# Kernel tuning notes

Hardware: AMD Instinct MI355X
Metric: run time of the kernel (lower is better)

Reference implementation:

```python
import jax, jax.numpy as jnp
import numpy as np

B, T, H, V = 64, 512, 300, 50257


def setup_inputs() -> dict:
    key = jax.random.key(0)
    k0, k1, k2, k3, k4 = jax.random.split(key, 5)
    tokens = jax.random.randint(k0, (B, T), 0, V, dtype=jnp.int32)
    ihs = jnp.zeros((B, H), jnp.float32)
    emb = jax.random.normal(k1, (V, H), jnp.float32) * 0.02
    W = jax.random.normal(k2, (H, H), jnp.float32) * (1.0 / np.sqrt(H))
    U = jax.random.normal(k3, (H, H), jnp.float32) * (1.0 / np.sqrt(H))
    Wout = jax.random.normal(k4, (V, H), jnp.float32) * 0.02
    bout = jnp.zeros((V,), jnp.float32)
    return {"ihs": ihs, "tokens": tokens, "emb": emb, "W": W, "U": U,
            "Wout": Wout, "bout": bout}


def reference(ihs, tokens, emb, W, U, Wout, bout):
    # Embedding lookup: [B, T, H]
    x = emb[tokens]
    # Precompute input projection for all timesteps: U x_t (Linear: x @ U^T)
    ux = jnp.einsum('bth,gh->btg', x, U)  # [B, T, H]
    ux_tmajor = jnp.swapaxes(ux, 0, 1)    # [T, B, H]

    def step(h, ux_t):
        # h_t = tanh(W h_{t-1} + U x_t)
        h_next = jnp.tanh(h @ W.T + ux_t)
        return h_next, h_next

    h_last, _ = jax.lax.scan(step, ihs, ux_tmajor)
    # final hidden state -> vocab logits
    logits = h_last @ Wout.T + bout  # [B, V]
    return logits
```

## Files before the change

kernel.cpp:

```cpp
#include <hip/hip_runtime.h>
#include <math.h>

#define H 300
#define BB 64
#define TT 512
#define VV 50257
#define KC 30

__global__ void transpose_k(const float* __restrict__ in, float* __restrict__ out) {
    int idx = blockIdx.x * blockDim.x + threadIdx.x;
    if (idx < H * H) {
        int r = idx / H, c = idx - r * H;
        out[idx] = in[c * H + r];
    }
}

__global__ __launch_bounds__(256) void ux_k(const int* __restrict__ tokens,
                                            const float* __restrict__ emb,
                                            const float* __restrict__ Ut,
                                            float* __restrict__ ux) {
    __shared__ __align__(16) float x_s[KC][BB];
    __shared__ __align__(16) float ut_s[KC][304];
    __shared__ int tok_s[BB];

    const int t = blockIdx.x;
    const int tid = threadIdx.x;
    if (tid < BB) tok_s[tid] = tokens[tid * TT + t];

    const int tb = tid >> 4;
    const int tg = tid & 15;
    const int b0 = tb * 4;
    const int g0 = tg * 20;
    const bool active = (tg < 15);

    float acc[4][20];
#pragma unroll
    for (int i = 0; i < 4; ++i)
#pragma unroll
        for (int j = 0; j < 20; ++j) acc[i][j] = 0.f;

    __syncthreads();

    for (int h0 = 0; h0 < H; h0 += KC) {
        for (int i = tid; i < BB * 32; i += 256) {
            int b = i >> 5, k = i & 31;
            if (k < KC) x_s[k][b] = emb[tok_s[b] * H + h0 + k];
        }
        for (int i = tid; i < KC * H; i += 256) {
            int k = i / H, g = i - k * H;
            ut_s[k][g] = Ut[(h0 + k) * H + g];
        }
        __syncthreads();
        if (active) {
#pragma unroll 2
            for (int k = 0; k < KC; ++k) {
                float4 xa = *reinterpret_cast<const float4*>(&x_s[k][b0]);
                float4 u0 = *reinterpret_cast<const float4*>(&ut_s[k][g0 + 0]);
                float4 u1 = *reinterpret_cast<const float4*>(&ut_s[k][g0 + 4]);
                float4 u2 = *reinterpret_cast<const float4*>(&ut_s[k][g0 + 8]);
                float4 u3 = *reinterpret_cast<const float4*>(&ut_s[k][g0 + 12]);
                float4 u4 = *reinterpret_cast<const float4*>(&ut_s[k][g0 + 16]);
                const float xr[4] = {xa.x, xa.y, xa.z, xa.w};
                const float ur[20] = {u0.x, u0.y, u0.z, u0.w,
                                      u1.x, u1.y, u1.z, u1.w,
                                      u2.x, u2.y, u2.z, u2.w,
                                      u3.x, u3.y, u3.z, u3.w,
                                      u4.x, u4.y, u4.z, u4.w};
#pragma unroll
                for (int i = 0; i < 4; ++i)
#pragma unroll
                    for (int j = 0; j < 20; ++j)
                        acc[i][j] += xr[i] * ur[j];
            }
        }
        __syncthreads();
    }

    if (active) {
#pragma unroll
        for (int i = 0; i < 4; ++i) {
            float* dst = ux + (t * BB + b0 + i) * H + g0;
#pragma unroll
            for (int jq = 0; jq < 5; ++jq) {
                *reinterpret_cast<float4*>(dst + jq * 4) =
                    make_float4(acc[i][jq * 4 + 0], acc[i][jq * 4 + 1],
                                acc[i][jq * 4 + 2], acc[i][jq * 4 + 3]);
            }
        }
    }
}

#define REP25(X) X(0) X(1) X(2) X(3) X(4) X(5) X(6) X(7) X(8) X(9) \
    X(10) X(11) X(12) X(13) X(14) X(15) X(16) X(17) X(18) X(19) \
    X(20) X(21) X(22) X(23) X(24)

__global__ __attribute__((amdgpu_flat_work_group_size(512, 512), amdgpu_waves_per_eu(2, 2)))
void rnn_k(const float* __restrict__ W,
           const float* __restrict__ ux,
           const float* __restrict__ ihs,
           float* __restrict__ hlast) {
    __shared__ __align__(16) float h_s[304];
    __shared__ float p_s[608];
    const int b = blockIdx.x;
    const int tid = threadIdx.x;
    const int tt = (tid < 450) ? tid : 449;
    const int c = tt / 150;
    const int g2 = tt - c * 150;

    const float* wr0 = W + (size_t)g2 * H + c * 100;
    const float* wr1 = W + (size_t)(g2 + 150) * H + c * 100;

#define WDECL(q) \
    float a##q##0 = wr0[4*q+0], a##q##1 = wr0[4*q+1], a##q##2 = wr0[4*q+2], a##q##3 = wr0[4*q+3]; \
    float b##q##0 = wr1[4*q+0], b##q##1 = wr1[4*q+1], b##q##2 = wr1[4*q+2], b##q##3 = wr1[4*q+3];
    REP25(WDECL)
#undef WDECL

    if (tid < H) h_s[tid] = ihs[b * H + tid];

    const float* uxb = ux + b * H;
    float u0 = 0.f, u1 = 0.f;
    if (tid < 150) {
        u0 = uxb[g2];
        u1 = uxb[150 + g2];
    }
    __syncthreads();

    const float4* hs4 = reinterpret_cast<const float4*>(h_s);
    const int hoff = c * 25;

#pragma unroll 1
    for (int t = 0; t < TT; ++t) {
        float n0 = 0.f, n1 = 0.f;
        if (tid < 150 && t + 1 < TT) {
            const float* nx = uxb + (t + 1) * (BB * H);
            n0 = nx[g2];
            n1 = nx[150 + g2];
        }
        float accA0 = 0.f, accA1 = 0.f, accA2 = 0.f, accA3 = 0.f;
        float accB0 = 0.f, accB1 = 0.f, accB2 = 0.f, accB3 = 0.f;
#define WSTEP(q) { float4 h4 = hs4[hoff + q]; \
        accA0 += a##q##0 * h4.x; accA1 += a##q##1 * h4.y; \
        accA2 += a##q##2 * h4.z; accA3 += a##q##3 * h4.w; \
        accB0 += b##q##0 * h4.x; accB1 += b##q##1 * h4.y; \
        accB2 += b##q##2 * h4.z; accB3 += b##q##3 * h4.w; }
        REP25(WSTEP)
#undef WSTEP
        float accA = (accA0 + accA1) + (accA2 + accA3);
        float accB = (accB0 + accB1) + (accB2 + accB3);
        if (tid < 450 && c == 1) { p_s[g2] = accA; p_s[150 + g2] = accB; }
        if (tid < 450 && c == 2) { p_s[304 + g2] = accA; p_s[454 + g2] = accB; }
        __syncthreads();
        if (tid < 150) {
            float z0 = accA + p_s[g2] + p_s[304 + g2] + u0;
            float z1 = accB + p_s[150 + g2] + p_s[454 + g2] + u1;
            float e0 = __expf(2.f * z0);
            float e1 = __expf(2.f * z1);
            h_s[g2]       = 1.f - 2.f * __builtin_amdgcn_rcpf(e0 + 1.f);
            h_s[150 + g2] = 1.f - 2.f * __builtin_amdgcn_rcpf(e1 + 1.f);
        }
        u0 = n0; u1 = n1;
        __syncthreads();
    }
    if (tid < H) hlast[b * H + tid] = h_s[tid];
}

__global__ __launch_bounds__(256) void logits_k(const float* __restrict__ hlast,
                                                const float* __restrict__ Wout,
                                                const float* __restrict__ bout,
                                                float* __restrict__ out) {
    __shared__ float hT[152 * 65];
    const int tid = threadIdx.x;
    const int lane = tid & 63;
    const int wv = tid >> 6;
    const int v0 = blockIdx.x * 64;
    const int vb0 = __builtin_amdgcn_readfirstlane(v0 + wv * 16);
    const float* wb = Wout + (size_t)vb0 * H;
    const bool full = (vb0 + 16 <= VV);

    float acc[16];
#pragma unroll
    for (int r = 0; r < 16; ++r) acc[r] = 0.f;

    for (int p = 0; p < 2; ++p) {
        const int hbase = p ? 148 : 0;
        const int hn = p ? 152 : 148;
        __syncthreads();
        for (int i = tid; i < BB * hn; i += 256) {
            int b = i / hn, h = i - b * hn;
            hT[h * 65 + b] = hlast[b * H + hbase + h];
        }
        __syncthreads();
        if (full) {
            for (int hc = 0; hc < hn; hc += 4) {
                float hv0 = hT[(hc + 0) * 65 + lane];
                float hv1 = hT[(hc + 1) * 65 + lane];
                float hv2 = hT[(hc + 2) * 65 + lane];
                float hv3 = hT[(hc + 3) * 65 + lane];
#pragma unroll
                for (int r = 0; r < 16; ++r) {
                    const float4 w4 = *reinterpret_cast<const float4*>(wb + r * H + hbase + hc);
                    acc[r] += hv0 * w4.x + hv1 * w4.y + hv2 * w4.z + hv3 * w4.w;
                }
            }
        } else {
            for (int hc = 0; hc < hn; hc += 4) {
                float hv0 = hT[(hc + 0) * 65 + lane];
                float hv1 = hT[(hc + 1) * 65 + lane];
                float hv2 = hT[(hc + 2) * 65 + lane];
                float hv3 = hT[(hc + 3) * 65 + lane];
#pragma unroll
                for (int r = 0; r < 16; ++r) {
                    int vr = vb0 + r; if (vr > VV - 1) vr = VV - 1;
                    const float4 w4 = *reinterpret_cast<const float4*>(
                        Wout + (size_t)vr * H + hbase + hc);
                    acc[r] += hv0 * w4.x + hv1 * w4.y + hv2 * w4.z + hv3 * w4.w;
                }
            }
        }
    }

    __syncthreads();
#pragma unroll
    for (int r = 0; r < 16; ++r) hT[(wv * 16 + r) * 65 + lane] = acc[r];
    __syncthreads();
#pragma unroll
    for (int k = 0; k < 16; ++k) {
        int i = tid + k * 256;
        int v = i & 63, bb = i >> 6;
        if (v0 + v < VV)
            out[(size_t)bb * VV + v0 + v] = hT[v * 65 + bb] + bout[v0 + v];
    }
}

extern "C" void kernel_launch(void* const* d_in, const int* in_sizes, int n_in,
                              void* d_out, int out_size, void* d_ws, size_t ws_size,
                              hipStream_t stream) {
    const float* ihs    = (const float*)d_in[0];
    const int*   tokens = (const int*)  d_in[1];
    const float* emb    = (const float*)d_in[2];
    const float* W      = (const float*)d_in[3];
    const float* U      = (const float*)d_in[4];
    const float* Wout   = (const float*)d_in[5];
    const float* bout   = (const float*)d_in[6];
    float* out = (float*)d_out;

    char* ws = (char*)d_ws;
    float* Ut    = (float*)(ws + 0);
    float* hlast = (float*)(ws + 400000);
    float* ux    = (float*)(ws + 1048576);

    const int tp_blocks = (H * H + 255) / 256;
    transpose_k<<<tp_blocks, 256, 0, stream>>>(U, Ut);
    ux_k<<<TT, 256, 0, stream>>>(tokens, emb, Ut, ux);
    rnn_k<<<BB, 512, 0, stream>>>(W, ux, ihs, hlast);
    logits_k<<<(VV + 63) / 64, 256, 0, stream>>>(hlast, Wout, bout, out);
}
```

Before: 855.7 us.

## Offload part of RNN weights to LDS and retile logits GEMM via shared memory

The recurrent kernel now keeps most W slices in registers and stores the last few float4 chunks per thread in LDS. This is meant to relieve register pressure and avoid spills under the 2-waves-per-EU constraint, at the cost of extra LDS reads on each serial timestep. The logits kernel is rewritten as a classic tiled GEMM: it stages 128-vocab by 32-hidden Wout tiles and transposed hidden tiles in shared memory, and each thread computes an 8x4 register tile. This is meant to improve coalescing and reuse of Wout.

```diff
diff --git a/kernel.cpp b/kernel.cpp
--- a/kernel.cpp
+++ b/kernel.cpp
@@ -90,15 +90,15 @@
     }
 }
 
-#define REP25(X) X(0) X(1) X(2) X(3) X(4) X(5) X(6) X(7) X(8) X(9) \
-    X(10) X(11) X(12) X(13) X(14) X(15) X(16) X(17) X(18) X(19) \
-    X(20) X(21) X(22) X(23) X(24)
+#define RNN_REP19(X) X(0) X(1) X(2) X(3) X(4) X(5) X(6) X(7) X(8) X(9) \
+    X(10) X(11) X(12) X(13) X(14) X(15) X(16) X(17) X(18)
 
 __global__ __attribute__((amdgpu_flat_work_group_size(512, 512), amdgpu_waves_per_eu(2, 2)))
 void rnn_k(const float* __restrict__ W,
            const float* __restrict__ ux,
            const float* __restrict__ ihs,
            float* __restrict__ hlast) {
+    __shared__ __align__(16) float4 wl4_s[450 * 11];
     __shared__ __align__(16) float h_s[304];
     __shared__ float p_s[608];
     const int b = blockIdx.x;
@@ -107,14 +107,22 @@
     const int c = tt / 150;
     const int g2 = tt - c * 150;
 
-    const float* wr0 = W + (size_t)g2 * H + c * 100;
-    const float* wr1 = W + (size_t)(g2 + 150) * H + c * 100;
-
-#define WDECL(q) \
-    float a##q##0 = wr0[4*q+0], a##q##1 = wr0[4*q+1], a##q##2 = wr0[4*q+2], a##q##3 = wr0[4*q+3]; \
-    float b##q##0 = wr1[4*q+0], b##q##1 = wr1[4*q+1], b##q##2 = wr1[4*q+2], b##q##3 = wr1[4*q+3];
-    REP25(WDECL)
-#undef WDECL
+    const float4* wrA4 = reinterpret_cast<const float4*>(W + (size_t)g2 * H + c * 100);
+    const float4* wrB4 = reinterpret_cast<const float4*>(W + (size_t)(g2 + 150) * H + c * 100);
+
+#define RNN_WA(q) float4 wa##q = wrA4[q];
+    RNN_REP19(RNN_WA)
+#undef RNN_WA
+#define RNN_WB(q) float4 wb##q = wrB4[q];
+    RNN_REP19(RNN_WB)
+#undef RNN_WB
+    float4 wb19 = wrB4[19];
+
+    const int wbase = tt * 11;
+#pragma unroll
+    for (int i = 0; i < 6; ++i) wl4_s[wbase + i] = wrA4[19 + i];
+#pragma unroll
+    for (int i = 0; i < 5; ++i) wl4_s[wbase + 6 + i] = wrB4[20 + i];
 
     if (tid < H) h_s[tid] = ihs[b * H + tid];
 
@@ -139,13 +147,31 @@
         }
         float accA0 = 0.f, accA1 = 0.f, accA2 = 0.f, accA3 = 0.f;
         float accB0 = 0.f, accB1 = 0.f, accB2 = 0.f, accB3 = 0.f;
-#define WSTEP(q) { float4 h4 = hs4[hoff + q]; \
-        accA0 += a##q##0 * h4.x; accA1 += a##q##1 * h4.y; \
-        accA2 += a##q##2 * h4.z; accA3 += a##q##3 * h4.w; \
-        accB0 += b##q##0 * h4.x; accB1 += b##q##1 * h4.y; \
-        accB2 += b##q##2 * h4.z; accB3 += b##q##3 * h4.w; }
-        REP25(WSTEP)
-#undef WSTEP
+#define RNN_Q(q) { float4 h4 = hs4[hoff + q]; \
+        accA0 += wa##q.x * h4.x; accA1 += wa##q.y * h4.y; \
+        accA2 += wa##q.z * h4.z; accA3 += wa##q.w * h4.w; \
+        accB0 += wb##q.x * h4.x; accB1 += wb##q.y * h4.y; \
+        accB2 += wb##q.z * h4.z; accB3 += wb##q.w * h4.w; }
+        RNN_REP19(RNN_Q)
+#undef RNN_Q
+        {
+            float4 h4 = hs4[hoff + 19];
+            float4 wA = wl4_s[wbase + 0];
+            accA0 += wA.x * h4.x; accA1 += wA.y * h4.y;
+            accA2 += wA.z * h4.z; accA3 += wA.w * h4.w;
+            accB0 += wb19.x * h4.x; accB1 += wb19.y * h4.y;
+            accB2 += wb19.z * h4.z; accB3 += wb19.w * h4.w;
+        }
+#pragma unroll
+        for (int q = 20; q < 25; ++q) {
+            float4 h4 = hs4[hoff + q];
+            float4 wA = wl4_s[wbase + (q - 19)];
+            float4 wB = wl4_s[wbase + 6 + (q - 20)];
+            accA0 += wA.x * h4.x; accA1 += wA.y * h4.y;
+            accA2 += wA.z * h4.z; accA3 += wA.w * h4.w;
+            accB0 += wB.x * h4.x; accB1 += wB.y * h4.y;
+            accB2 += wB.z * h4.z; accB3 += wB.w * h4.w;
+        }
         float accA = (accA0 + accA1) + (accA2 + accA3);
         float accB = (accB0 + accB1) + (accB2 + accB3);
         if (tid < 450 && c == 1) { p_s[g2] = accA; p_s[150 + g2] = accB; }
@@ -169,67 +195,103 @@
                                                 const float* __restrict__ Wout,
                                                 const float* __restrict__ bout,
                                                 float* __restrict__ out) {
-    __shared__ float hT[152 * 65];
+    __shared__ __align__(16) float Ws[32 * 132];
+    __shared__ __align__(16) float hs[32 * 76];
     const int tid = threadIdx.x;
-    const int lane = tid & 63;
-    const int wv = tid >> 6;
-    const int v0 = blockIdx.x * 64;
-    const int vb0 = __builtin_amdgcn_readfirstlane(v0 + wv * 16);
-    const float* wb = Wout + (size_t)vb0 * H;
-    const bool full = (vb0 + 16 <= VV);
-
-    float acc[16];
-#pragma unroll
-    for (int r = 0; r < 16; ++r) acc[r] = 0.f;
-
-    for (int p = 0; p < 2; ++p) {
-        const int hbase = p ? 148 : 0;
-        const int hn = p ? 152 : 148;
-        __syncthreads();
-        for (int i = tid; i < BB * hn; i += 256) {
-            int b = i / hn, h = i - b * hn;
-            hT[h * 65 + b] = hlast[b * H + hbase + h];
-        }
-        __syncthreads();
-        if (full) {
-            for (int hc = 0; hc < hn; hc += 4) {
-                float hv0 = hT[(hc + 0) * 65 + lane];
-                float hv1 = hT[(hc + 1) * 65 + lane];
-                float hv2 = hT[(hc + 2) * 65 + lane];
-                float hv3 = hT[(hc + 3) * 65 + lane];
-#pragma unroll
-                for (int r = 0; r < 16; ++r) {
-                    const float4 w4 = *reinterpret_cast<const float4*>(wb + r * H + hbase + hc);
-                    acc[r] += hv0 * w4.x + hv1 * w4.y + hv2 * w4.z + hv3 * w4.w;
+    const int tv = tid & 31;
+    const int tb = tid >> 5;
+    const int v0 = blockIdx.x * 128;
+
+    float acc[8][4];
+#pragma unroll
+    for (int i = 0; i < 8; ++i)
+#pragma unroll
+        for (int j = 0; j < 4; ++j) acc[i][j] = 0.f;
+
+    for (int hb = 0; hb < H; hb += 32) {
+        __syncthreads();
+        {
+            const int vp = tid >> 1;
+            const int hloc = (tid & 1) * 16;
+            int vv = v0 + vp; if (vv > VV - 1) vv = VV - 1;
+            const float* wrow = Wout + (size_t)vv * H + hb + hloc;
+#pragma unroll
+            for (int i = 0; i < 4; ++i) {
+                const int hg = hb + hloc + i * 4;
+                float4 val;
+                if (hg + 3 < H) {
+                    val = *reinterpret_cast<const float4*>(wrow + i * 4);
+                } else {
+                    val.x = (hg + 0 < H) ? wrow[i * 4 + 0] : 0.f;
+                    val.y = (hg + 1 < H) ? wrow[i * 4 + 1] : 0.f;
+                    val.z = (hg + 2 < H) ? wrow[i * 4 + 2] : 0.f;
+                    val.w = (hg + 3 < H) ? wrow[i * 4 + 3] : 0.f;
                 }
-            }
-        } else {
-            for (int hc = 0; hc < hn; hc += 4) {
-                float hv0 = hT[(hc + 0) * 65 + lane];
-                float hv1 = hT[(hc + 1) * 65 + lane];
-                float hv2 = hT[(hc + 2) * 65 + lane];
-                float hv3 = hT[(hc + 3) * 65 + lane];
-#pragma unroll
-                for (int r = 0; r < 16; ++r) {
-                    int vr = vb0 + r; if (vr > VV - 1) vr = VV - 1;
-                    const float4 w4 = *reinterpret_cast<const float4*>(
-                        Wout + (size_t)vr * H + hbase + hc);
-                    acc[r] += hv0 * w4.x + hv1 * w4.y + hv2 * w4.z + hv3 * w4.w;
+                Ws[(hloc + i * 4 + 0) * 132 + vp] = val.x;
+                Ws[(hloc + i * 4 + 1) * 132 + vp] = val.y;
+                Ws[(hloc + i * 4 + 2) * 132 + vp] = val.z;
+                Ws[(hloc + i * 4 + 3) * 132 + vp] = val.w;
+            }
+        }
+        {
+            const int bb = tid >> 2;
+            const int hl = (tid & 3) * 8;
+            const float* hrow = hlast + bb * H + hb + hl;
+#pragma unroll
+            for (int i = 0; i < 2; ++i) {
+                const int hg = hb + hl + i * 4;
+                float4 val;
+                if (hg + 3 < H) {
+                    val = *reinterpret_cast<const float4*>(hrow + i * 4);
+                } else {
+                    val.x = (hg + 0 < H) ? hrow[i * 4 + 0] : 0.f;
+                    val.y = (hg + 1 < H) ? hrow[i * 4 + 1] : 0.f;
+                    val.z = (hg + 2 < H) ? hrow[i * 4 + 2] : 0.f;
+                    val.w = (hg + 3 < H) ? hrow[i * 4 + 3] : 0.f;
                 }
-            }
-        }
-    }
-
-    __syncthreads();
-#pragma unroll
-    for (int r = 0; r < 16; ++r) hT[(wv * 16 + r) * 65 + lane] = acc[r];
-    __syncthreads();
-#pragma unroll
-    for (int k = 0; k < 16; ++k) {
-        int i = tid + k * 256;
-        int v = i & 63, bb = i >> 6;
-        if (v0 + v < VV)
-            out[(size_t)bb * VV + v0 + v] = hT[v * 65 + bb] + bout[v0 + v];
+                hs[(hl + i * 4 + 0) * 76 + bb] = val.x;
+                hs[(hl + i * 4 + 1) * 76 + bb] = val.y;
+                hs[(hl + i * 4 + 2) * 76 + bb] = val.z;
+                hs[(hl + i * 4 + 3) * 76 + bb] = val.w;
+            }
+        }
+        __syncthreads();
+        const float4* Ws4 = reinterpret_cast<const float4*>(Ws);
+        const float4* hs4 = reinterpret_cast<const float4*>(hs);
+#pragma unroll
+        for (int h2 = 0; h2 < 32; ++h2) {
+            float4 w4  = Ws4[h2 * 33 + tv];
+            float4 h4a = hs4[h2 * 19 + tb * 2];
+            float4 h4b = hs4[h2 * 19 + tb * 2 + 1];
+            const float hv[8] = {h4a.x, h4a.y, h4a.z, h4a.w,
+                                 h4b.x, h4b.y, h4b.z, h4b.w};
+#pragma unroll
+            for (int bi = 0; bi < 8; ++bi) {
+                acc[bi][0] += hv[bi] * w4.x;
+                acc[bi][1] += hv[bi] * w4.y;
+                acc[bi][2] += hv[bi] * w4.z;
+                acc[bi][3] += hv[bi] * w4.w;
+            }
+        }
+    }
+
+    const int vg = v0 + tv * 4;
+    float4 bq;
+    if (vg + 3 < VV) bq = *reinterpret_cast<const float4*>(bout + vg);
+    else {
+        bq.x = (vg + 0 < VV) ? bout[vg + 0] : 0.f;
+        bq.y = (vg + 1 < VV) ? bout[vg + 1] : 0.f;
+        bq.z = (vg + 2 < VV) ? bout[vg + 2] : 0.f;
+        bq.w = (vg + 3 < VV) ? bout[vg + 3] : 0.f;
+    }
+#pragma unroll
+    for (int bi = 0; bi < 8; ++bi) {
+        const int bb = tb * 8 + bi;
+        float* op = out + (size_t)bb * VV + vg;
+        if (vg + 0 < VV) op[0] = acc[bi][0] + bq.x;
+        if (vg + 1 < VV) op[1] = acc[bi][1] + bq.y;
+        if (vg + 2 < VV) op[2] = acc[bi][2] + bq.z;
+        if (vg + 3 < VV) op[3] = acc[bi][3] + bq.w;
     }
 }
 
@@ -254,5 +316,5 @@
     transpose_k<<<tp_blocks, 256, 0, stream>>>(U, Ut);
     ux_k<<<TT, 256, 0, stream>>>(tokens, emb, Ut, ux);
     rnn_k<<<BB, 512, 0, stream>>>(W, ux, ihs, hlast);
-    logits_k<<<(VV + 63) / 64, 256, 0, stream>>>(hlast, Wout, bout, out);
-}
+    logits_k<<<(VV + 127) / 128, 256, 0, stream>>>(hlast, Wout, bout, out);
+}
```

New measurement: 811.5 us. 5.2% less time.
